# Performance work log

Measured on AMD Instinct MI355X. Metric: run time of the kernel, lower is better.

The kernel has to match this reference:

```python
import jax, jax.numpy as jnp
import numpy as np
import math


def setup_inputs() -> dict:
    key = jax.random.key(0)
    ks = jax.random.split(key, 4)
    B, C, H, W, D = 16, 512, 64, 64, 256
    return {
        "x": jax.random.normal(ks[0], (B, C, H, W), jnp.float32),
        "weight_global": jax.random.normal(ks[1], (C, D), jnp.float32) * 0.02,  # trunc_normal std=0.02
        "conv_g_w": jax.random.normal(ks[2], (C, C), jnp.float32) * 0.02,       # 1x1 conv, no bias
        "bn_g_gamma": jnp.ones((C,), jnp.float32),
        "bn_g_beta": jnp.zeros((C,), jnp.float32),
        "conv_c_w": jax.random.normal(ks[3], (C, C), jnp.float32) * 0.02,
        "bn_c_gamma": jnp.ones((C,), jnp.float32),
        "bn_c_beta": jnp.zeros((C,), jnp.float32),
    }


def _bn(x, gamma, beta, eps=1e-5):
    # BatchNorm2d in default training mode: batch statistics over (B, H, W)
    mean = x.mean(axis=(0, 2, 3), keepdims=True)
    var = x.var(axis=(0, 2, 3), keepdims=True)
    xn = (x - mean) * jax.lax.rsqrt(var + eps)
    return xn * gamma[None, :, None, None] + beta[None, :, None, None]


def reference(x, weight_global, conv_g_w, bn_g_gamma, bn_g_beta, conv_c_w, bn_c_gamma, bn_c_beta):
    b, c, h, w = x.shape
    inv_sqrt_c = 1.0 / math.sqrt(c)

    # Description: QR-orthogonal codebook, Q: (c, d)
    Q, _ = jnp.linalg.qr(weight_global + 1e-8)

    # global branch: 1x1 conv -> BN -> ReLU -> global avg pool
    gx = jnp.einsum('oc,bchw->bohw', conv_g_w, x)
    gx = jax.nn.relu(_bn(gx, bn_g_gamma, bn_g_beta))
    g = gx.mean(axis=(2, 3))                                  # (b, c)
    aff_g = jax.nn.softmax((g @ Q) * inv_sqrt_c, axis=1)      # (b, d)
    g = jax.nn.sigmoid(aff_g @ Q.T)                           # (b, c)

    # channel branch: 1x1 conv -> BN -> ReLU
    cx = jnp.einsum('oc,bchw->bohw', conv_c_w, x)
    cx = jax.nn.relu(_bn(cx, bn_c_gamma, bn_c_beta))
    ch = cx.reshape(b, c, h * w).transpose(0, 2, 1)           # (b, hw, c)
    aff_c = jax.nn.softmax((ch @ Q) * inv_sqrt_c, axis=2)     # (b, hw, d)
    # sum(diag_embed(aff_c) @ Q.T, dim=2) == aff_c @ Q.T (fused, avoids (b,hw,d,c) intermediate)
    ch = aff_c @ Q.T                                          # (b, hw, c)

    o = ch * g[:, None, :]
    o = o.transpose(0, 2, 1).reshape(b, c, h, w)
    return o + x
```

## Files before the change

### kernel.cpp

```cpp
#include <hip/hip_runtime.h>
#include <hip/hip_bf16.h>

#define BB 16
#define CC 512
#define HWP 4096
#define DD 256
#define NPIX 65536
#define INV_SQRT_C 0.04419417382415922f

typedef unsigned short u16;
typedef __attribute__((ext_vector_type(8))) short s16x8;
typedef __attribute__((ext_vector_type(8))) unsigned short u16x8;
typedef __attribute__((ext_vector_type(4))) unsigned short u16x4;
typedef __attribute__((ext_vector_type(4))) float f32x4;

__device__ __forceinline__ u16 f2b(float f){
  unsigned int u = __builtin_bit_cast(unsigned int, f);
  unsigned int r = (u + 0x7fffu + ((u >> 16) & 1u)) >> 16;
  return (u16)r;
}

__device__ __forceinline__ f32x4 mfma16(s16x8 a, s16x8 b, f32x4 c){
  return __builtin_amdgcn_mfma_f32_16x16x32_bf16(a, b, c, 0, 0, 0);
}

__global__ __launch_bounds__(256) void k_xbar(const float* __restrict__ x, float* __restrict__ xbar){
  int c = blockIdx.x, tid = threadIdx.x;
  float s = 0.f;
  for (int b = 0; b < BB; ++b){
    const float* px = x + ((size_t)(b*CC + c))*HWP;
    for (int p = tid; p < HWP; p += 256) s += px[p];
  }
  __shared__ float red[256];
  red[tid] = s; __syncthreads();
  for (int st = 128; st; st >>= 1){ if (tid < st) red[tid] += red[tid+st]; __syncthreads(); }
  if (tid == 0) xbar[c] = red[0] * (1.0f/ (float)NPIX);
}

__global__ __launch_bounds__(512) void k_gram(const float* __restrict__ x, float* __restrict__ Spart, int kspl){
  __shared__ __align__(16) u16 Asl[128*72];
  __shared__ __align__(16) u16 Bsl[128*72];
  int tid = threadIdx.x;
  int w = tid >> 6, lane = tid & 63, lr = lane & 15, g = lane >> 4;
  int b = blockIdx.y;
  int kz = blockIdx.z;
  int t = blockIdx.x, ti = 0, rem = 4;
  while (t >= rem){ t -= rem; ++ti; --rem; }
  int tj = ti + t;
  int r0 = ti*128, c0 = tj*128;
  int wm = w >> 2, wn = w & 3;
  f32x4 acc[4][2] = {};
  const float* xb = x + (size_t)b*CC*HWP;
  int klen = HWP / kspl;
  int kbase = kz * klen;
  for (int k0 = kbase; k0 < kbase + klen; k0 += 64){
    __syncthreads();
    for (int tt = tid; tt < 4096; tt += 512){
      int arr = tt >> 11;
      int row = (tt >> 4) & 127;
      int q = tt & 15;
      const float* src = xb + (size_t)((arr ? c0 : r0) + row)*HWP + k0 + q*4;
      f32x4 v = *(const f32x4*)src;
      u16x4 u; u[0]=f2b(v[0]); u[1]=f2b(v[1]); u[2]=f2b(v[2]); u[3]=f2b(v[3]);
      u16* dst = (arr ? Bsl : Asl) + row*72 + q*4;
      *(u16x4*)dst = u;
    }
    __syncthreads();
    #pragma unroll
    for (int kc = 0; kc < 2; ++kc){
      s16x8 av[4], bv[2];
      #pragma unroll
      for (int mt = 0; mt < 4; ++mt) av[mt] = *(const s16x8*)&Asl[(wm*64 + mt*16 + lr)*72 + kc*32 + g*8];
      #pragma unroll
      for (int nt = 0; nt < 2; ++nt) bv[nt] = *(const s16x8*)&Bsl[(wn*32 + nt*16 + lr)*72 + kc*32 + g*8];
      #pragma unroll
      for (int mt = 0; mt < 4; ++mt)
        #pragma unroll
        for (int nt = 0; nt < 2; ++nt)
          acc[mt][nt] = mfma16(av[mt], bv[nt], acc[mt][nt]);
    }
  }
  float* sp = Spart + (size_t)(b*kspl + kz)*262144;
  #pragma unroll
  for (int mt = 0; mt < 4; ++mt)
    #pragma unroll
    for (int nt = 0; nt < 2; ++nt)
      #pragma unroll
      for (int r = 0; r < 4; ++r)
        sp[(size_t)(r0 + wm*64 + mt*16 + 4*g + r)*512 + c0 + wn*32 + nt*16 + lr] = acc[mt][nt][r];
}

__global__ __launch_bounds__(256) void k_sreduce(const float* __restrict__ Spart, float* __restrict__ S, int nslots){
  int idx = blockIdx.x*256 + threadIdx.x;
  int i = idx >> 9, j = idx & 511;
  int src = ((i >> 7) <= (j >> 7)) ? idx : (j*512 + i);
  float s = 0.f;
  for (int k = 0; k < nslots; ++k) s += Spart[(size_t)k*262144 + src];
  S[idx] = s;
}

__global__ __launch_bounds__(256) void k_G(const float* __restrict__ wg, float* __restrict__ G){
  int i = blockIdx.x, j = threadIdx.x;
  float s = 0.f;
  for (int c = 0; c < CC; ++c)
    s = fmaf(wg[c*DD + i] + 1e-8f, wg[c*DD + j] + 1e-8f, s);
  G[i*DD + j] = s;
}

__global__ __launch_bounds__(256) void k_cholPanel(float* __restrict__ G, int kb){
  int tid = threadIdx.x;
  int lane = tid & 63;
  int j = lane & 31;
  int K0 = kb*32;
  float c[32];
  #pragma unroll
  for (int i = 0; i < 32; ++i)
    c[i] = (i <= j) ? G[(K0+i)*DD + K0 + j] : 0.f;
  #pragma unroll
  for (int k = 0; k < 32; ++k){
    float piv = __shfl(c[k], k);
    float sd = sqrtf(piv);
    float ukj = c[k] / sd;
    c[k] = ukj;
    float uk[32];
    #pragma unroll
    for (int i = k + 1; i < 32; ++i) uk[i] = __shfl(ukj, i);
    #pragma unroll
    for (int i = k + 1; i < 32; ++i) c[i] -= uk[i] * ukj;
  }
  if (tid < 32){
    #pragma unroll
    for (int i = 0; i < 32; ++i)
      if (i <= j) G[(K0+i)*DD + K0 + j] = c[i];
  }
  int nt = 256 - K0 - 32;
  int jg = K0 + 32 + tid;
  if (tid < nt){
    float y[32];
    #pragma unroll
    for (int i = 0; i < 32; ++i) y[i] = G[(K0+i)*DD + jg];
    #pragma unroll
    for (int i = 0; i < 32; ++i){
      float s0 = y[i];
      #pragma unroll
      for (int l = 0; l < 32; ++l)
        if (l < i) s0 -= __shfl(c[l], i) * y[l];
      y[i] = s0 / __shfl(c[i], i);
    }
    #pragma unroll
    for (int i = 0; i < 32; ++i) G[(K0+i)*DD + jg] = y[i];
  }
}

__global__ __launch_bounds__(256) void k_cholTrail(float* __restrict__ G, int kb){
  int K0 = kb*32;
  int nt = 256 - K0 - 32;
  int T = (nt + 63) >> 6;
  int t = blockIdx.x, ti = 0, rem = T;
  while (t >= rem){ t -= rem; ++ti; --rem; }
  int tj = ti + t;
  int r0 = K0 + 32 + ti*64;
  int c0 = K0 + 32 + tj*64;
  __shared__ __align__(16) float Ur[32][64];
  __shared__ __align__(16) float Uc[32][64];
  int tid = threadIdx.x;
  for (int idx = tid; idx < 2048; idx += 256){
    int k = idx >> 6, cc = idx & 63;
    int gr = r0 + cc, gc = c0 + cc;
    Ur[k][cc] = (gr < 256) ? G[(K0+k)*DD + gr] : 0.f;
    Uc[k][cc] = (gc < 256) ? G[(K0+k)*DD + gc] : 0.f;
  }
  __syncthreads();
  int tr = (tid >> 4) * 4;
  int tc = (tid & 15) * 4;
  float acc[4][4] = {};
  #pragma unroll
  for (int k = 0; k < 32; ++k){
    f32x4 a = *(const f32x4*)&Ur[k][tr];
    f32x4 b = *(const f32x4*)&Uc[k][tc];
    #pragma unroll
    for (int ii = 0; ii < 4; ++ii)
      #pragma unroll
      for (int jj = 0; jj < 4; ++jj)
        acc[ii][jj] += a[ii]*b[jj];
  }
  #pragma unroll
  for (int ii = 0; ii < 4; ++ii){
    int gi = r0 + tr + ii;
    if (gi >= 256) continue;
    #pragma unroll
    for (int jj = 0; jj < 4; ++jj){
      int gj = c0 + tc + jj;
      if (gj < 256 && gj >= gi)
        G[gi*DD + gj] -= acc[ii][jj];
    }
  }
}

__global__ __launch_bounds__(256) void k_qsolve(const float* __restrict__ G,
    const float* __restrict__ wg,
    float* __restrict__ Q, float* __restrict__ Qst,
    u16* __restrict__ Qb, u16* __restrict__ Qstb){
  __shared__ __align__(16) float Pp[8192];
  __shared__ float Qlds[256*64];
  __shared__ float Wred[3*32*64];
  int tid = threadIdx.x;
  int w = tid >> 6, lane = tid & 63;
  int c = blockIdx.x*64 + lane;
  const float* arow = wg + (size_t)c*DD;

  for (int J = 0; J < 8; ++J){
    int J0 = J*32;
    int nrows8 = (J0 + 32)*8;
    for (int idx = tid; idx < nrows8; idx += 256){
      int row = idx >> 3, q = idx & 7;
      *(f32x4*)&Pp[row*32 + q*4] = *(const f32x4*)&G[row*256 + J0 + q*4];
    }
    __syncthreads();

    float W[32];
    if (w == 0){
      #pragma unroll
      for (int r = 0; r < 32; ++r) W[r] = arow[J0 + r] + 1e-8f;
    } else {
      #pragma unroll
      for (int r = 0; r < 32; ++r) W[r] = 0.f;
    }
    for (int M = w; M < J; M += 4){
      #pragma unroll 4
      for (int k = 0; k < 32; ++k){
        int row = M*32 + k;
        float qv = Qlds[row*64 + lane];
        const float* pr = &Pp[row*32];
        #pragma unroll
        for (int r4 = 0; r4 < 8; ++r4){
          f32x4 p = *(const f32x4*)&pr[r4*4];
          W[r4*4+0] -= qv*p[0];
          W[r4*4+1] -= qv*p[1];
          W[r4*4+2] -= qv*p[2];
          W[r4*4+3] -= qv*p[3];
        }
      }
    }
    if (w > 0){
      #pragma unroll
      for (int r = 0; r < 32; ++r) Wred[((w-1)*32 + r)*64 + lane] = W[r];
    }
    __syncthreads();

    if (w == 0){
      #pragma unroll
      for (int r = 0; r < 32; ++r)
        W[r] += Wred[r*64 + lane] + Wred[(32+r)*64 + lane] + Wred[(64+r)*64 + lane];
      #pragma unroll
      for (int i = 0; i < 32; ++i){
        float t = W[i];
        for (int l = 0; l < i; ++l) t -= W[l] * Pp[(J0 + l)*32 + i];
        W[i] = t / Pp[(J0 + i)*32 + i];
      }
      #pragma unroll
      for (int i = 0; i < 32; ++i) Qlds[(J0 + i)*64 + lane] = W[i];
      #pragma unroll
      for (int r4 = 0; r4 < 8; ++r4){
        f32x4 q4; u16x4 qb4;
        #pragma unroll
        for (int jj = 0; jj < 4; ++jj){ q4[jj] = W[r4*4+jj]; qb4[jj] = f2b(W[r4*4+jj]); }
        *(f32x4*)&Q[(size_t)c*DD + J0 + r4*4] = q4;
        *(u16x4*)&Qb[(size_t)c*DD + J0 + r4*4] = qb4;
      }
      #pragma unroll
      for (int i = 0; i < 32; ++i){
        float qs = W[i] * INV_SQRT_C;
        Qst[(size_t)(J0 + i)*CC + c] = qs;
        Qstb[(size_t)(J0 + i)*CC + c] = f2b(qs);
      }
    }
    __syncthreads();
  }
}

__global__ __launch_bounds__(256) void k_fold(const float* __restrict__ Wg, const float* __restrict__ Wc,
    const float* __restrict__ gamg, const float* __restrict__ betg,
    const float* __restrict__ gamc, const float* __restrict__ betc,
    const float* __restrict__ S, const float* __restrict__ xbar,
    float* __restrict__ Wgf, float* __restrict__ bgf,
    float* __restrict__ Wcf, float* __restrict__ bcf,
    u16* __restrict__ Wgb, u16* __restrict__ Wcb){
  int o = blockIdx.x & 511, br = blockIdx.x >> 9;
  int tid = threadIdx.x;
  const float* W = br ? Wc : Wg;
  __shared__ float wrow[512];
  __shared__ float red[256];
  __shared__ float red2[256];
  __shared__ float sc_s, bi_s;
  wrow[tid] = W[o*512 + tid]; wrow[tid+256] = W[o*512 + tid + 256];
  __syncthreads();
  float mp = 0.f;
  for (int c = tid; c < 512; c += 256) mp = fmaf(wrow[c], xbar[c], mp);
  float qp = 0.f;
  for (int c1 = tid; c1 < 512; c1 += 256){
    const float* srow = S + (size_t)c1*512;
    float y = 0.f;
    for (int c2 = 0; c2 < 512; ++c2) y = fmaf(srow[c2], wrow[c2], y);
    qp = fmaf(wrow[c1], y, qp);
  }
  red[tid] = mp; red2[tid] = qp; __syncthreads();
  for (int st = 128; st; st >>= 1){
    if (tid < st){ red[tid] += red[tid+st]; red2[tid] += red2[tid+st]; }
    __syncthreads();
  }
  if (tid == 0){
    float m = red[0];
    float E = red2[0] * (1.0f/(float)NPIX);
    float var = E - m*m;
    float rstd = rsqrtf(var + 1e-5f);
    float gma = br ? gamc[o] : gamg[o];
    float bta = br ? betc[o] : betg[o];
    sc_s = gma * rstd;
    bi_s = bta - gma * rstd * m;
  }
  __syncthreads();
  float* Wf = br ? Wcf : Wgf;
  float* bf = br ? bcf : bgf;
  u16* Wb  = br ? Wcb : Wgb;
  float w0 = sc_s * wrow[tid], w1 = sc_s * wrow[tid+256];
  Wf[o*512 + tid]     = w0;
  Wf[o*512 + tid+256] = w1;
  Wb[o*512 + tid]     = f2b(w0);
  Wb[o*512 + tid+256] = f2b(w1);
  if (tid == 0) bf[o] = bi_s;
}

__global__ __launch_bounds__(512) void k_gconv(const float* __restrict__ x,
    const u16* __restrict__ Wb, const float* __restrict__ bf, float* __restrict__ gpart){
  __shared__ __align__(16) u16 Xs[64*512];
  int tid = threadIdx.x;
  int w = tid >> 6, lane = tid & 63, lr = lane & 15, g = lane >> 4;
  int slab = blockIdx.x, b = blockIdx.y;
  int p0 = slab*64;

  {
    const float* xb = x + (size_t)b*CC*HWP + p0;
    int p = tid & 63;
    int c8 = (tid >> 6) * 8;
    for (int pass = 0; pass < 8; ++pass, c8 += 64){
      float v[8];
      #pragma unroll
      for (int i = 0; i < 8; ++i) v[i] = xb[(size_t)(c8 + i)*HWP + p];
      u16x8 u;
      #pragma unroll
      for (int i = 0; i < 8; ++i) u[i] = f2b(v[i]);
      *(u16x8*)&Xs[p*512 + (c8 ^ ((p & 7) << 3))] = u;
    }
  }
  __syncthreads();

  for (int i = 0; i < 4; ++i){
    int o0 = (w*4 + i)*16;
    f32x4 acc[4] = {};
    for (int k = 0; k < 16; ++k){
      int c0 = k*32 + g*8;
      s16x8 a = *(const s16x8*)(Wb + (size_t)(o0 + lr)*512 + c0);
      #pragma unroll
      for (int pt = 0; pt < 4; ++pt){
        int p = pt*16 + lr;
        s16x8 bv = *(const s16x8*)&Xs[p*512 + (c0 ^ ((p & 7) << 3))];
        acc[pt] = mfma16(a, bv, acc[pt]);
      }
    }
    f32x4 bias4 = *(const f32x4*)(bf + o0 + 4*g);
    float s[4] = {0.f, 0.f, 0.f, 0.f};
    #pragma unroll
    for (int pt = 0; pt < 4; ++pt)
      #pragma unroll
      for (int r = 0; r < 4; ++r)
        s[r] += fmaxf(acc[pt][r] + bias4[r], 0.f);
    #pragma unroll
    for (int r = 0; r < 4; ++r){
      s[r] += __shfl_xor(s[r], 1);
      s[r] += __shfl_xor(s[r], 2);
      s[r] += __shfl_xor(s[r], 4);
      s[r] += __shfl_xor(s[r], 8);
    }
    if (lr == 0){
      f32x4 sv; sv[0]=s[0]; sv[1]=s[1]; sv[2]=s[2]; sv[3]=s[3];
      *(f32x4*)(gpart + (size_t)(b*64 + slab)*512 + o0 + 4*g) = sv;
    }
  }
}

__global__ __launch_bounds__(256) void k_gvec(const float* __restrict__ gpart, const float* __restrict__ Q,
    const float* __restrict__ Qst, float* __restrict__ gvec){
  int b = blockIdx.x, tid = threadIdx.x;
  __shared__ float g0[512];
  __shared__ float aff[256];
  __shared__ float red[256];
  for (int o = tid; o < 512; o += 256){
    float s = 0.f;
    for (int sl = 0; sl < 64; ++sl) s += gpart[(size_t)(b*64 + sl)*512 + o];
    g0[o] = s * (1.0f/4096.0f);
  }
  __syncthreads();
  float l = 0.f;
  { const float* qr = Qst + (size_t)tid*512;
    for (int c = 0; c < 512; ++c) l = fmaf(qr[c], g0[c], l); }
  red[tid] = l; __syncthreads();
  for (int st = 128; st; st >>= 1){ if (tid < st) red[tid] = fmaxf(red[tid], red[tid+st]); __syncthreads(); }
  float m = red[0]; __syncthreads();
  float e = expf(l - m);
  red[tid] = e; __syncthreads();
  for (int st = 128; st; st >>= 1){ if (tid < st) red[tid] += red[tid+st]; __syncthreads(); }
  float inv = 1.0f/red[0];
  aff[tid] = e * inv;
  __syncthreads();
  for (int o = tid; o < 512; o += 256){
    const float* qr = Q + (size_t)o*DD;
    float v = 0.f;
    for (int d = 0; d < DD; ++d) v = fmaf(aff[d], qr[d], v);
    gvec[b*512 + o] = 1.0f/(1.0f + expf(-v));
  }
}

__global__ __launch_bounds__(512) void k_fused(const float* __restrict__ x,
    const u16* __restrict__ Wcb, const float* __restrict__ bcf,
    const u16* __restrict__ Qstb, const u16* __restrict__ Qb,
    const float* __restrict__ gvec, float* __restrict__ out){
  __shared__ __align__(16) u16 Xs[64*512];
  __shared__ __align__(16) u16 Ts[64*512];
  float* Lsf = (float*)Xs;
  u16*   As  = Ts;
  int tid = threadIdx.x;
  int w = tid >> 6, lane = tid & 63, lr = lane & 15, g = lane >> 4;
  int b = blockIdx.y, p0 = blockIdx.x*64;

  {
    const float* xb = x + (size_t)b*CC*HWP + p0;
    int p = tid & 63;
    int c8 = (tid >> 6) * 8;
    for (int pass = 0; pass < 8; ++pass, c8 += 64){
      float v[8];
      #pragma unroll
      for (int i = 0; i < 8; ++i) v[i] = xb[(size_t)(c8 + i)*HWP + p];
      u16x8 u;
      #pragma unroll
      for (int i = 0; i < 8; ++i) u[i] = f2b(v[i]);
      *(u16x8*)&Xs[p*512 + (c8 ^ ((p & 7) << 3))] = u;
    }
  }
  __syncthreads();

  for (int i = 0; i < 4; ++i){
    int o0 = (w*4 + i)*16;
    f32x4 acc[4] = {};
    for (int k = 0; k < 16; ++k){
      int c0 = k*32 + g*8;
      s16x8 a = *(const s16x8*)(Wcb + (size_t)(o0 + lr)*512 + c0);
      #pragma unroll
      for (int pt = 0; pt < 4; ++pt){
        int p = pt*16 + lr;
        s16x8 bv = *(const s16x8*)&Xs[p*512 + (c0 ^ ((p & 7) << 3))];
        acc[pt] = mfma16(a, bv, acc[pt]);
      }
    }
    f32x4 bias4 = *(const f32x4*)(bcf + o0 + 4*g);
    #pragma unroll
    for (int pt = 0; pt < 4; ++pt){
      int p = pt*16 + lr;
      u16x4 u;
      #pragma unroll
      for (int r = 0; r < 4; ++r) u[r] = f2b(fmaxf(acc[pt][r] + bias4[r], 0.f));
      *(u16x4*)&Ts[p*512 + ((o0 + 4*g) ^ ((p & 7) << 3))] = u;
    }
  }
  __syncthreads();

  for (int i = 0; i < 2; ++i){
    int d0 = (w*2 + i)*16;
    f32x4 acc[4] = {};
    for (int k = 0; k < 16; ++k){
      int o0 = k*32 + g*8;
      s16x8 a = *(const s16x8*)(Qstb + (size_t)(d0 + lr)*512 + o0);
      #pragma unroll
      for (int pt = 0; pt < 4; ++pt){
        int p = pt*16 + lr;
        s16x8 bv = *(const s16x8*)&Ts[p*512 + (o0 ^ ((p & 7) << 3))];
        acc[pt] = mfma16(a, bv, acc[pt]);
      }
    }
    #pragma unroll
    for (int pt = 0; pt < 4; ++pt){
      int p = pt*16 + lr;
      *(f32x4*)&Lsf[p*256 + ((d0 + 4*g) ^ ((p & 7) << 2))] = acc[pt];
    }
  }
  __syncthreads();

  {
    int px = tid >> 3, sub = tid & 7;
    float* Lrow = Lsf + px*256;
    int sw2 = (px & 7) << 2, sw3 = (px & 7) << 3;
    float v[32];
    #pragma unroll
    for (int jj = 0; jj < 8; ++jj){
      int d0 = sub*32 + jj*4;
      f32x4 t = *(const f32x4*)&Lrow[d0 ^ sw2];
      v[jj*4+0] = t[0]; v[jj*4+1] = t[1]; v[jj*4+2] = t[2]; v[jj*4+3] = t[3];
    }
    float m = v[0];
    #pragma unroll
    for (int jj = 1; jj < 32; ++jj) m = fmaxf(m, v[jj]);
    m = fmaxf(m, __shfl_xor(m, 1));
    m = fmaxf(m, __shfl_xor(m, 2));
    m = fmaxf(m, __shfl_xor(m, 4));
    float s = 0.f;
    #pragma unroll
    for (int jj = 0; jj < 32; ++jj){ v[jj] = __expf(v[jj] - m); s += v[jj]; }
    s += __shfl_xor(s, 1);
    s += __shfl_xor(s, 2);
    s += __shfl_xor(s, 4);
    float inv = 1.0f/s;
    #pragma unroll
    for (int jj = 0; jj < 4; ++jj){
      int d0 = sub*32 + jj*8;
      u16x8 u;
      #pragma unroll
      for (int i = 0; i < 8; ++i) u[i] = f2b(v[jj*8+i] * inv);
      *(u16x8*)&As[px*256 + (d0 ^ sw3)] = u;
    }
  }
  __syncthreads();

  for (int i = 0; i < 4; ++i){
    int o0 = (w*4 + i)*16;
    f32x4 acc[4] = {};
    for (int k = 0; k < 8; ++k){
      int d0 = k*32 + g*8;
      s16x8 a = *(const s16x8*)(Qb + (size_t)(o0 + lr)*256 + d0);
      #pragma unroll
      for (int pt = 0; pt < 4; ++pt){
        int p = pt*16 + lr;
        s16x8 bv = *(const s16x8*)&As[p*256 + (d0 ^ ((p & 7) << 3))];
        acc[pt] = mfma16(a, bv, acc[pt]);
      }
    }
    f32x4 gg = *(const f32x4*)(gvec + b*512 + o0 + 4*g);
    #pragma unroll
    for (int pt = 0; pt < 4; ++pt){
      #pragma unroll
      for (int r = 0; r < 4; ++r){
        size_t idx = (size_t)(b*CC + o0 + 4*g + r)*HWP + p0 + pt*16 + lr;
        out[idx] = fmaf(acc[pt][r], gg[r], x[idx]);
      }
    }
  }
}

extern "C" void kernel_launch(void* const* d_in, const int* in_sizes, int n_in,
                              void* d_out, int out_size, void* d_ws, size_t ws_size,
                              hipStream_t stream) {
  const float* x    = (const float*)d_in[0];
  const float* wg   = (const float*)d_in[1];
  const float* Wg   = (const float*)d_in[2];
  const float* gamg = (const float*)d_in[3];
  const float* betg = (const float*)d_in[4];
  const float* Wc   = (const float*)d_in[5];
  const float* gamc = (const float*)d_in[6];
  const float* betc = (const float*)d_in[7];
  float* out = (float*)d_out;

  int kspl = 1;
  {
    size_t need2 = ((size_t)1320448 + 2*16*262144 + 524288 + 393216) * 4;
    if (ws_size >= need2) kspl = 2;
  }

  float* ws = (float*)d_ws;
  float* G     = ws + 0;
  float* Q     = ws + 131072;
  float* Qst   = ws + 262144;
  float* S     = ws + 393216;
  float* xbar  = ws + 655360;
  float* Wgf   = ws + 655872;
  float* bgf   = ws + 918016;
  float* Wcf   = ws + 918528;
  float* bcf   = ws + 1180672;
  float* gvec  = ws + 1181184;
  float* Spart = ws + 1320448;
  float* gpart = Spart + (size_t)kspl*16*262144;
  u16*   ub    = (u16*)(gpart + 524288);
  u16* Qb   = ub;
  u16* Qstb = ub + 131072;
  u16* Wgb  = ub + 262144;
  u16* Wcb  = ub + 524288;

  k_xbar<<<512, 256, 0, stream>>>(x, xbar);
  k_gram<<<dim3(10,16,kspl), 512, 0, stream>>>(x, Spart, kspl);
  k_sreduce<<<1024, 256, 0, stream>>>(Spart, S, 16*kspl);
  k_G<<<256, 256, 0, stream>>>(wg, G);
  for (int kb = 0; kb < 8; ++kb){
    k_cholPanel<<<1, 256, 0, stream>>>(G, kb);
    int nt = 256 - kb*32 - 32;
    if (nt > 0){
      int T = (nt + 63) >> 6;
      k_cholTrail<<<T*(T+1)/2, 256, 0, stream>>>(G, kb);
    }
  }
  k_qsolve<<<8, 256, 0, stream>>>(G, wg, Q, Qst, Qb, Qstb);
  k_fold<<<1024, 256, 0, stream>>>(Wg, Wc, gamg, betg, gamc, betc, S, xbar, Wgf, bgf, Wcf, bcf, Wgb, Wcb);
  k_gconv<<<dim3(64,16), 512, 0, stream>>>(x, Wgb, bgf, gpart);
  k_gvec<<<16, 256, 0, stream>>>(gpart, Q, Qst, gvec);
  k_fused<<<dim3(64,16), 512, 0, stream>>>(x, Wcb, bcf, Qstb, Qb, gvec, out);
}
```

Before: 1.022 ms.

## Hoist LDS B-fragment loads across output tiles with 4x4 register accumulator blocking

Reorders the MFMA loops in the global-branch, channel-branch and output GEMMs so the k loop is outermost. Each LDS B fragment is loaded once per k step and reused across all output-row tiles, instead of being reloaded for every tile. This cuts LDS read traffic by up to 4x and gives the scheduler more independent MFMAs to interleave. In exchange it holds up to 16 f32x4 accumulators live per thread, which raises register pressure and may lower occupancy or cause spills.

Result: faster. 964.1 us (-5.6%).

```diff
diff --git a/kernel.cpp b/kernel.cpp
--- a/kernel.cpp
+++ b/kernel.cpp
@@ -355,26 +355,34 @@
   }
   __syncthreads();
 
+  f32x4 acc[4][4] = {};
+  for (int k = 0; k < 16; ++k){
+    int c0 = k*32 + g*8;
+    s16x8 bv[4];
+    #pragma unroll
+    for (int pt = 0; pt < 4; ++pt){
+      int p = pt*16 + lr;
+      bv[pt] = *(const s16x8*)&Xs[p*512 + (c0 ^ ((p & 7) << 3))];
+    }
+    #pragma unroll
+    for (int i = 0; i < 4; ++i){
+      int o0 = (w*4 + i)*16;
+      s16x8 a = *(const s16x8*)(Wb + (size_t)(o0 + lr)*512 + c0);
+      #pragma unroll
+      for (int pt = 0; pt < 4; ++pt)
+        acc[i][pt] = mfma16(a, bv[pt], acc[i][pt]);
+    }
+  }
+  #pragma unroll
   for (int i = 0; i < 4; ++i){
     int o0 = (w*4 + i)*16;
-    f32x4 acc[4] = {};
-    for (int k = 0; k < 16; ++k){
-      int c0 = k*32 + g*8;
-      s16x8 a = *(const s16x8*)(Wb + (size_t)(o0 + lr)*512 + c0);
-      #pragma unroll
-      for (int pt = 0; pt < 4; ++pt){
-        int p = pt*16 + lr;
-        s16x8 bv = *(const s16x8*)&Xs[p*512 + (c0 ^ ((p & 7) << 3))];
-        acc[pt] = mfma16(a, bv, acc[pt]);
-      }
-    }
     f32x4 bias4 = *(const f32x4*)(bf + o0 + 4*g);
     float s[4] = {0.f, 0.f, 0.f, 0.f};
     #pragma unroll
     for (int pt = 0; pt < 4; ++pt)
       #pragma unroll
       for (int r = 0; r < 4; ++r)
-        s[r] += fmaxf(acc[pt][r] + bias4[r], 0.f);
+        s[r] += fmaxf(acc[i][pt][r] + bias4[r], 0.f);
     #pragma unroll
     for (int r = 0; r < 4; ++r){
       s[r] += __shfl_xor(s[r], 1);
@@ -449,48 +457,68 @@
   }
   __syncthreads();
 
-  for (int i = 0; i < 4; ++i){
-    int o0 = (w*4 + i)*16;
-    f32x4 acc[4] = {};
+  {
+    f32x4 acc[4][4] = {};
     for (int k = 0; k < 16; ++k){
       int c0 = k*32 + g*8;
-      s16x8 a = *(const s16x8*)(Wcb + (size_t)(o0 + lr)*512 + c0);
+      s16x8 bv[4];
       #pragma unroll
       for (int pt = 0; pt < 4; ++pt){
         int p = pt*16 + lr;
-        s16x8 bv = *(const s16x8*)&Xs[p*512 + (c0 ^ ((p & 7) << 3))];
-        acc[pt] = mfma16(a, bv, acc[pt]);
-      }
-    }
-    f32x4 bias4 = *(const f32x4*)(bcf + o0 + 4*g);
-    #pragma unroll
-    for (int pt = 0; pt < 4; ++pt){
-      int p = pt*16 + lr;
-      u16x4 u;
-      #pragma unroll
-      for (int r = 0; r < 4; ++r) u[r] = f2b(fmaxf(acc[pt][r] + bias4[r], 0.f));
-      *(u16x4*)&Ts[p*512 + ((o0 + 4*g) ^ ((p & 7) << 3))] = u;
-    }
-  }
-  __syncthreads();
-
-  for (int i = 0; i < 2; ++i){
-    int d0 = (w*2 + i)*16;
-    f32x4 acc[4] = {};
+        bv[pt] = *(const s16x8*)&Xs[p*512 + (c0 ^ ((p & 7) << 3))];
+      }
+      #pragma unroll
+      for (int i = 0; i < 4; ++i){
+        int o0 = (w*4 + i)*16;
+        s16x8 a = *(const s16x8*)(Wcb + (size_t)(o0 + lr)*512 + c0);
+        #pragma unroll
+        for (int pt = 0; pt < 4; ++pt)
+          acc[i][pt] = mfma16(a, bv[pt], acc[i][pt]);
+      }
+    }
+    #pragma unroll
+    for (int i = 0; i < 4; ++i){
+      int o0 = (w*4 + i)*16;
+      f32x4 bias4 = *(const f32x4*)(bcf + o0 + 4*g);
+      #pragma unroll
+      for (int pt = 0; pt < 4; ++pt){
+        int p = pt*16 + lr;
+        u16x4 u;
+        #pragma unroll
+        for (int r = 0; r < 4; ++r) u[r] = f2b(fmaxf(acc[i][pt][r] + bias4[r], 0.f));
+        *(u16x4*)&Ts[p*512 + ((o0 + 4*g) ^ ((p & 7) << 3))] = u;
+      }
+    }
+  }
+  __syncthreads();
+
+  {
+    f32x4 acc[2][4] = {};
     for (int k = 0; k < 16; ++k){
       int o0 = k*32 + g*8;
-      s16x8 a = *(const s16x8*)(Qstb + (size_t)(d0 + lr)*512 + o0);
+      s16x8 bv[4];
       #pragma unroll
       for (int pt = 0; pt < 4; ++pt){
         int p = pt*16 + lr;
-        s16x8 bv = *(const s16x8*)&Ts[p*512 + (o0 ^ ((p & 7) << 3))];
-        acc[pt] = mfma16(a, bv, acc[pt]);
-      }
-    }
-    #pragma unroll
-    for (int pt = 0; pt < 4; ++pt){
-      int p = pt*16 + lr;
-      *(f32x4*)&Lsf[p*256 + ((d0 + 4*g) ^ ((p & 7) << 2))] = acc[pt];
+        bv[pt] = *(const s16x8*)&Ts[p*512 + (o0 ^ ((p & 7) << 3))];
+      }
+      #pragma unroll
+      for (int i = 0; i < 2; ++i){
+        int d0 = (w*2 + i)*16;
+        s16x8 a = *(const s16x8*)(Qstb + (size_t)(d0 + lr)*512 + o0);
+        #pragma unroll
+        for (int pt = 0; pt < 4; ++pt)
+          acc[i][pt] = mfma16(a, bv[pt], acc[i][pt]);
+      }
+    }
+    #pragma unroll
+    for (int i = 0; i < 2; ++i){
+      int d0 = (w*2 + i)*16;
+      #pragma unroll
+      for (int pt = 0; pt < 4; ++pt){
+        int p = pt*16 + lr;
+        *(f32x4*)&Lsf[p*256 + ((d0 + 4*g) ^ ((p & 7) << 2))] = acc[i][pt];
+      }
     }
   }
   __syncthreads();
@@ -530,26 +558,36 @@
   }
   __syncthreads();
 
-  for (int i = 0; i < 4; ++i){
-    int o0 = (w*4 + i)*16;
-    f32x4 acc[4] = {};
+  {
+    f32x4 acc[4][4] = {};
     for (int k = 0; k < 8; ++k){
       int d0 = k*32 + g*8;
-      s16x8 a = *(const s16x8*)(Qb + (size_t)(o0 + lr)*256 + d0);
+      s16x8 bv[4];
       #pragma unroll
       for (int pt = 0; pt < 4; ++pt){
         int p = pt*16 + lr;
-        s16x8 bv = *(const s16x8*)&As[p*256 + (d0 ^ ((p & 7) << 3))];
-        acc[pt] = mfma16(a, bv, acc[pt]);
-      }
-    }
-    f32x4 gg = *(const f32x4*)(gvec + b*512 + o0 + 4*g);
-    #pragma unroll
-    for (int pt = 0; pt < 4; ++pt){
-      #pragma unroll
-      for (int r = 0; r < 4; ++r){
-        size_t idx = (size_t)(b*CC + o0 + 4*g + r)*HWP + p0 + pt*16 + lr;
-        out[idx] = fmaf(acc[pt][r], gg[r], x[idx]);
+        bv[pt] = *(const s16x8*)&As[p*256 + (d0 ^ ((p & 7) << 3))];
+      }
+      #pragma unroll
+      for (int i = 0; i < 4; ++i){
+        int o0 = (w*4 + i)*16;
+        s16x8 a = *(const s16x8*)(Qb + (size_t)(o0 + lr)*256 + d0);
+        #pragma unroll
+        for (int pt = 0; pt < 4; ++pt)
+          acc[i][pt] = mfma16(a, bv[pt], acc[i][pt]);
+      }
+    }
+    #pragma unroll
+    for (int i = 0; i < 4; ++i){
+      int o0 = (w*4 + i)*16;
+      f32x4 gg = *(const f32x4*)(gvec + b*512 + o0 + 4*g);
+      #pragma unroll
+      for (int pt = 0; pt < 4; ++pt){
+        #pragma unroll
+        for (int r = 0; r < 4; ++r){
+          size_t idx = (size_t)(b*CC + o0 + 4*g + r)*HWP + p0 + pt*16 + lr;
+          out[idx] = fmaf(acc[i][pt][r], gg[r], x[idx]);
+        }
       }
     }
   }
```
